# Kernel tuning notes

Measured on AMD Instinct MI355X. Metric: run time of the kernel, lower is better.

The kernel has to match this reference:

```python
import jax, jax.numpy as jnp
import numpy as np

B, H, S, DK = 4, 8, 2048, 64

def setup_inputs() -> dict:
    key = jax.random.key(0)
    kq, kk, kv = jax.random.split(key, 3)
    queries = jax.random.normal(kq, (B, H, S, DK), dtype=jnp.float32)
    keys = jax.random.normal(kk, (B, H, S, DK), dtype=jnp.float32)
    values = jax.random.normal(kv, (B, H, S, DK), dtype=jnp.float32)
    # causal mask: 1.0 where attention is disallowed (strictly upper triangular)
    mask = jnp.triu(jnp.ones((S, S), dtype=jnp.float32), k=1)[None, None]
    return {"queries": queries, "keys": keys, "values": values, "dk": DK, "mask": mask}

def reference(queries, keys, values, dk, mask):
    # score: [B, H, S, S]
    score = jnp.einsum("bhqd,bhkd->bhqk", queries, keys) / jnp.sqrt(jnp.float32(dk))
    if mask is not None:
        score = score + mask * -1e9
    attn = jax.nn.softmax(score, axis=-1)
    return jnp.einsum("bhqk,bhkd->bhqd", attn, values)
```

## Files before the change

### kernel.cpp

```cpp
#include <hip/hip_runtime.h>

typedef __attribute__((ext_vector_type(8))) short short8;
typedef __attribute__((ext_vector_type(4))) float f32x4;

#define DEV __device__ __forceinline__

constexpr int S_LEN = 2048;
constexpr int DK_LEN = 64;
constexpr int KBLK = 64;
constexpr float QSCALE = 0.18033688011112042f;

constexpr int KHI = 0;
constexpr int KLO = 8192;
constexpr int VHI = 16384;
constexpr int VLO = 24576;
constexpr int PBASE = 32768;
constexpr int LDS_BYTES = 65536;

DEV unsigned int f2bf(float x) {
  unsigned int u = __float_as_uint(x);
  return (u + 0x7fffu + ((u >> 16) & 1u)) >> 16;
}
DEV float bf2f(unsigned int h) { return __uint_as_float(h << 16); }
DEV int swz(int row, int slot) { return slot ^ ((row + (row >> 3)) & 7); }

DEV f32x4 MFMA(short8 a, short8 b, f32x4 c) {
  return __builtin_amdgcn_mfma_f32_16x16x32_bf16(a, b, c, 0, 0, 0);
}

__global__ __launch_bounds__(256, 2)
void fattn_fwd(const float* __restrict__ Qg, const float* __restrict__ Kg,
               const float* __restrict__ Vg, float* __restrict__ Og)
{
  __shared__ char smem[LDS_BYTES];
  const f32x4 vzero = {0.f, 0.f, 0.f, 0.f};
  const int tid = threadIdx.x;
  const int w  = tid >> 6;
  const int ln = tid & 63;
  const int g  = ln >> 4;
  const int c  = ln & 15;
  const int bh = blockIdx.y;
  const int j  = blockIdx.x;
  const int hc = 31 - j;
  const int lc = j;
  int qb[2];
  qb[0] = hc * 64 + 16 * w;
  qb[1] = lc * 64 + 16 * w;
  const size_t base = (size_t)bh * S_LEN * DK_LEN;
  const float* Qb = Qg + base;
  const float* Kb = Kg + base;
  const float* Vb = Vg + base;

  short8 qfh[2][2], qfl[2][2];
#pragma unroll
  for (int qt = 0; qt < 2; ++qt) {
    const float* Qr = Qb + (size_t)(qb[qt] + c) * DK_LEN;
#pragma unroll
    for (int kk = 0; kk < 2; ++kk) {
      f32x4 a = *(const f32x4*)(Qr + kk * 32 + 8 * g);
      f32x4 b = *(const f32x4*)(Qr + kk * 32 + 8 * g + 4);
      float x[8];
#pragma unroll
      for (int i = 0; i < 4; ++i) { x[i] = a[i] * QSCALE; x[4 + i] = b[i] * QSCALE; }
#pragma unroll
      for (int i = 0; i < 8; ++i) {
        unsigned int h = f2bf(x[i]);
        unsigned int l = f2bf(x[i] - bf2f(h));
        qfh[qt][kk][i] = (short)h;
        qfl[qt][kk][i] = (short)l;
      }
    }
  }

  f32x4 acc[4][2];
#pragma unroll
  for (int td = 0; td < 4; ++td)
#pragma unroll
    for (int qt = 0; qt < 2; ++qt) acc[td][qt] = vzero;
  float m_r[2]  = {-3e38f, -3e38f};
  float lsum[2] = {0.f, 0.f};
  f32x4 sv[2][4];
  char* pw = smem + PBASE + w * 8192;

  auto softmax_store = [&](int qt) {
    float mt = -3e38f;
#pragma unroll
    for (int t = 0; t < 4; ++t)
#pragma unroll
      for (int r = 0; r < 4; ++r) mt = fmaxf(mt, sv[qt][t][r]);
    mt = fmaxf(mt, __shfl_xor(mt, 16));
    mt = fmaxf(mt, __shfl_xor(mt, 32));
    float mn = fmaxf(m_r[qt], mt);
    float sc = exp2f(m_r[qt] - mn);
    m_r[qt] = mn;
#pragma unroll
    for (int td = 0; td < 4; ++td) acc[td][qt] *= sc;
    float ps = 0.f;
    int qrow = 16 * qt + c;
    char* ph = pw + qrow * 128;
    char* pl = ph + 4096;
#pragma unroll
    for (int t = 0; t < 4; ++t) {
      float p[4];
#pragma unroll
      for (int r = 0; r < 4; ++r) { p[r] = exp2f(sv[qt][t][r] - mn); ps += p[r]; }
      unsigned int h0 = f2bf(p[0]), h1 = f2bf(p[1]), h2 = f2bf(p[2]), h3 = f2bf(p[3]);
      unsigned int l0 = f2bf(p[0] - bf2f(h0)), l1 = f2bf(p[1] - bf2f(h1));
      unsigned int l2 = f2bf(p[2] - bf2f(h2)), l3 = f2bf(p[3] - bf2f(h3));
      int kb = 32 * t + 8 * g;
      int byte = swz(qrow, kb >> 4) * 16 + (kb & 15);
      *(unsigned int*)(ph + byte)     = h0 | (h1 << 16);
      *(unsigned int*)(ph + byte + 4) = h2 | (h3 << 16);
      *(unsigned int*)(pl + byte)     = l0 | (l1 << 16);
      *(unsigned int*)(pl + byte + 4) = l2 | (l3 << 16);
    }
    lsum[qt] = lsum[qt] * sc + ps;
  };

  const int ntiles = hc + 1;
  for (int kt = 0; kt < ntiles; ++kt) {
    const int kv0 = kt * KBLK;
    __syncthreads();
#pragma unroll
    for (int i = 0; i < 4; ++i) {
      int f = tid + 256 * i;
      int row = f >> 4, c4 = f & 15;
      f32x4 kv = *(const f32x4*)(Kb + (size_t)(kv0 + row) * DK_LEN + c4 * 4);
      unsigned int h[4], l[4];
#pragma unroll
      for (int jj = 0; jj < 4; ++jj) { h[jj] = f2bf(kv[jj]); l[jj] = f2bf(kv[jj] - bf2f(h[jj])); }
      int byte = row * 128 + swz(row, c4 >> 1) * 16 + (c4 & 1) * 8;
      *(uint2*)(smem + KHI + byte) = make_uint2(h[0] | (h[1] << 16), h[2] | (h[3] << 16));
      *(uint2*)(smem + KLO + byte) = make_uint2(l[0] | (l[1] << 16), l[2] | (l[3] << 16));
    }
#pragma unroll
    for (int it = 0; it < 2; ++it) {
      int p = tid + 256 * it;
      int rp = p >> 4, c4 = p & 15;
      const float* vp = Vb + (size_t)(kv0 + 2 * rp) * DK_LEN + c4 * 4;
      f32x4 v0 = *(const f32x4*)(vp);
      f32x4 v1 = *(const f32x4*)(vp + DK_LEN);
#pragma unroll
      for (int jj = 0; jj < 4; ++jj) {
        int d = 4 * c4 + jj;
        unsigned int h0 = f2bf(v0[jj]), h1 = f2bf(v1[jj]);
        unsigned int l0 = f2bf(v0[jj] - bf2f(h0)), l1 = f2bf(v1[jj] - bf2f(h1));
        int byte = d * 128 + swz(d, rp >> 2) * 16 + (rp & 3) * 4;
        *(unsigned int*)(smem + VHI + byte) = h0 | (h1 << 16);
        *(unsigned int*)(smem + VLO + byte) = l0 | (l1 << 16);
      }
    }
    __syncthreads();

    const bool act1 = (kv0 <= qb[1] + 15);
    const bool nm0  = (kv0 + KBLK - 1) > qb[0];
    const bool nm1  = (kv0 + KBLK - 1) > qb[1];

#pragma unroll
    for (int qt = 0; qt < 2; ++qt)
#pragma unroll
      for (int t = 0; t < 4; ++t) sv[qt][t] = vzero;
#pragma unroll
    for (int t = 0; t < 4; ++t) {
      int row = 16 * t + c;
#pragma unroll
      for (int kk = 0; kk < 2; ++kk) {
        int off = row * 128 + swz(row, 4 * kk + g) * 16;
        short8 kh = *(const short8*)(smem + KHI + off);
        short8 kl = *(const short8*)(smem + KLO + off);
        sv[0][t] = MFMA(kh, qfh[0][kk], sv[0][t]);
        sv[0][t] = MFMA(kh, qfl[0][kk], sv[0][t]);
        sv[0][t] = MFMA(kl, qfh[0][kk], sv[0][t]);
        if (act1) {
          sv[1][t] = MFMA(kh, qfh[1][kk], sv[1][t]);
          sv[1][t] = MFMA(kh, qfl[1][kk], sv[1][t]);
          sv[1][t] = MFMA(kl, qfh[1][kk], sv[1][t]);
        }
      }
    }
    if (nm0) {
      int q = qb[0] + c;
#pragma unroll
      for (int t = 0; t < 4; ++t)
#pragma unroll
        for (int r = 0; r < 4; ++r)
          if (kv0 + 16 * t + 4 * g + r > q) sv[0][t][r] = -1e38f;
    }
    if (act1 && nm1) {
      int q = qb[1] + c;
#pragma unroll
      for (int t = 0; t < 4; ++t)
#pragma unroll
        for (int r = 0; r < 4; ++r)
          if (kv0 + 16 * t + 4 * g + r > q) sv[1][t][r] = -1e38f;
    }

    softmax_store(0);
    if (act1) softmax_store(1);

    short8 pbh[2][2], pbl[2][2];
#pragma unroll
    for (int kk = 0; kk < 2; ++kk) {
      int qrow = c;
      int off = qrow * 128 + swz(qrow, 4 * kk + g) * 16;
      pbh[0][kk] = *(const short8*)(pw + off);
      pbl[0][kk] = *(const short8*)(pw + 4096 + off);
    }
    if (act1) {
#pragma unroll
      for (int kk = 0; kk < 2; ++kk) {
        int qrow = 16 + c;
        int off = qrow * 128 + swz(qrow, 4 * kk + g) * 16;
        pbh[1][kk] = *(const short8*)(pw + off);
        pbl[1][kk] = *(const short8*)(pw + 4096 + off);
      }
    }
#pragma unroll
    for (int td = 0; td < 4; ++td) {
      int d = 16 * td + c;
#pragma unroll
      for (int kk = 0; kk < 2; ++kk) {
        int off = d * 128 + swz(d, 4 * kk + g) * 16;
        short8 vh = *(const short8*)(smem + VHI + off);
        short8 vl = *(const short8*)(smem + VLO + off);
        acc[td][0] = MFMA(vh, pbh[0][kk], acc[td][0]);
        acc[td][0] = MFMA(vh, pbl[0][kk], acc[td][0]);
        acc[td][0] = MFMA(vl, pbh[0][kk], acc[td][0]);
        if (act1) {
          acc[td][1] = MFMA(vh, pbh[1][kk], acc[td][1]);
          acc[td][1] = MFMA(vh, pbl[1][kk], acc[td][1]);
          acc[td][1] = MFMA(vl, pbh[1][kk], acc[td][1]);
        }
      }
    }
  }

#pragma unroll
  for (int qt = 0; qt < 2; ++qt) {
    float l = lsum[qt];
    l += __shfl_xor(l, 16);
    l += __shfl_xor(l, 32);
    float inv = 1.f / l;
    float* Ob = Og + base + (size_t)(qb[qt] + c) * DK_LEN;
#pragma unroll
    for (int td = 0; td < 4; ++td) {
      f32x4 o = acc[td][qt] * inv;
      *(f32x4*)(Ob + 16 * td + 4 * g) = o;
    }
  }
}

extern "C" void kernel_launch(void* const* d_in, const int* in_sizes, int n_in,
                              void* d_out, int out_size, void* d_ws, size_t ws_size,
                              hipStream_t stream) {
  (void)in_sizes; (void)n_in; (void)d_ws; (void)ws_size; (void)out_size;
  const float* Q = (const float*)d_in[0];
  const float* K = (const float*)d_in[1];
  const float* V = (const float*)d_in[2];
  float* O = (float*)d_out;
  dim3 grid(16, 32);
  fattn_fwd<<<grid, dim3(256), 0, stream>>>(Q, K, V, O);
}
```

Before: 208.7 us.

## Precompute split-bf16 K/V tile images once and stream them into LDS

Adds a prep kernel that converts K and V once per call into swizzled hi/lo bf16 tile images in the workspace. The attention kernel then copies each 32KB tile straight into LDS with global_load_lds instead of converting fp32 K/V itself in every block. This removes the conversion work that each of the 16 query blocks per head was repeating. In exchange it costs an extra launch and a workspace write/read, and it only runs if the workspace is at least 32MB; otherwise the old path is used.

```diff
diff --git a/kernel.cpp b/kernel.cpp
--- a/kernel.cpp
+++ b/kernel.cpp
@@ -14,6 +14,7 @@
 constexpr int KLO = 8192;
 constexpr int VHI = 16384;
 constexpr int VLO = 24576;
+constexpr int TILE_IMG = 32768;
 constexpr int PBASE = 32768;
 constexpr int LDS_BYTES = 65536;
 
@@ -28,9 +29,61 @@
   return __builtin_amdgcn_mfma_f32_16x16x32_bf16(a, b, c, 0, 0, 0);
 }
 
+DEV void gload_lds16(const void* g, void* l) {
+  __builtin_amdgcn_global_load_lds(
+      (const __attribute__((address_space(1))) unsigned int*)g,
+      (__attribute__((address_space(3))) unsigned int*)l, 16, 0, 0);
+}
+
+__global__ __launch_bounds__(256)
+void prep_kv(const float* __restrict__ Kg, const float* __restrict__ Vg,
+             char* __restrict__ ws)
+{
+  const int tid = threadIdx.x;
+  const int kt  = blockIdx.x;
+  const int bh  = blockIdx.y;
+  const int kv0 = kt * KBLK;
+  const size_t base = (size_t)bh * S_LEN * DK_LEN;
+  const float* Kb = Kg + base;
+  const float* Vb = Vg + base;
+  char* wt = ws + ((size_t)bh * 32 + kt) * TILE_IMG;
+
+#pragma unroll
+  for (int i = 0; i < 4; ++i) {
+    int f = tid + 256 * i;
+    int row = f >> 4, c4 = f & 15;
+    f32x4 kv = *(const f32x4*)(Kb + (size_t)(kv0 + row) * DK_LEN + c4 * 4);
+    unsigned int h[4], l[4];
+#pragma unroll
+    for (int j = 0; j < 4; ++j) { h[j] = f2bf(kv[j]); l[j] = f2bf(kv[j] - bf2f(h[j])); }
+    int byte = row * 128 + swz(row, c4 >> 1) * 16 + (c4 & 1) * 8;
+    *(uint2*)(wt + KHI + byte) = make_uint2(h[0] | (h[1] << 16), h[2] | (h[3] << 16));
+    *(uint2*)(wt + KLO + byte) = make_uint2(l[0] | (l[1] << 16), l[2] | (l[3] << 16));
+  }
+#pragma unroll
+  for (int it = 0; it < 2; ++it) {
+    int p = tid + 256 * it;
+    int rp = p >> 4, c4 = p & 15;
+    const float* vp = Vb + (size_t)(kv0 + 2 * rp) * DK_LEN + c4 * 4;
+    f32x4 v0 = *(const f32x4*)(vp);
+    f32x4 v1 = *(const f32x4*)(vp + DK_LEN);
+#pragma unroll
+    for (int j = 0; j < 4; ++j) {
+      int d = 4 * c4 + j;
+      unsigned int h0 = f2bf(v0[j]), h1 = f2bf(v1[j]);
+      unsigned int l0 = f2bf(v0[j] - bf2f(h0)), l1 = f2bf(v1[j] - bf2f(h1));
+      int byte = d * 128 + swz(d, rp >> 2) * 16 + (rp & 3) * 4;
+      *(unsigned int*)(wt + VHI + byte) = h0 | (h1 << 16);
+      *(unsigned int*)(wt + VLO + byte) = l0 | (l1 << 16);
+    }
+  }
+}
+
+template<bool PRE>
 __global__ __launch_bounds__(256, 2)
 void fattn_fwd(const float* __restrict__ Qg, const float* __restrict__ Kg,
-               const float* __restrict__ Vg, float* __restrict__ Og)
+               const float* __restrict__ Vg, float* __restrict__ Og,
+               const char* __restrict__ ws)
 {
   __shared__ char smem[LDS_BYTES];
   const f32x4 vzero = {0.f, 0.f, 0.f, 0.f};
@@ -50,6 +103,7 @@
   const float* Qb = Qg + base;
   const float* Kb = Kg + base;
   const float* Vb = Vg + base;
+  const char* wsb = ws + (size_t)bh * 32 * TILE_IMG;
 
   short8 qfh[2][2], qfl[2][2];
 #pragma unroll
@@ -121,33 +175,40 @@
   for (int kt = 0; kt < ntiles; ++kt) {
     const int kv0 = kt * KBLK;
     __syncthreads();
-#pragma unroll
-    for (int i = 0; i < 4; ++i) {
-      int f = tid + 256 * i;
-      int row = f >> 4, c4 = f & 15;
-      f32x4 kv = *(const f32x4*)(Kb + (size_t)(kv0 + row) * DK_LEN + c4 * 4);
-      unsigned int h[4], l[4];
-#pragma unroll
-      for (int jj = 0; jj < 4; ++jj) { h[jj] = f2bf(kv[jj]); l[jj] = f2bf(kv[jj] - bf2f(h[jj])); }
-      int byte = row * 128 + swz(row, c4 >> 1) * 16 + (c4 & 1) * 8;
-      *(uint2*)(smem + KHI + byte) = make_uint2(h[0] | (h[1] << 16), h[2] | (h[3] << 16));
-      *(uint2*)(smem + KLO + byte) = make_uint2(l[0] | (l[1] << 16), l[2] | (l[3] << 16));
-    }
-#pragma unroll
-    for (int it = 0; it < 2; ++it) {
-      int p = tid + 256 * it;
-      int rp = p >> 4, c4 = p & 15;
-      const float* vp = Vb + (size_t)(kv0 + 2 * rp) * DK_LEN + c4 * 4;
-      f32x4 v0 = *(const f32x4*)(vp);
-      f32x4 v1 = *(const f32x4*)(vp + DK_LEN);
-#pragma unroll
-      for (int jj = 0; jj < 4; ++jj) {
-        int d = 4 * c4 + jj;
-        unsigned int h0 = f2bf(v0[jj]), h1 = f2bf(v1[jj]);
-        unsigned int l0 = f2bf(v0[jj] - bf2f(h0)), l1 = f2bf(v1[jj] - bf2f(h1));
-        int byte = d * 128 + swz(d, rp >> 2) * 16 + (rp & 3) * 4;
-        *(unsigned int*)(smem + VHI + byte) = h0 | (h1 << 16);
-        *(unsigned int*)(smem + VLO + byte) = l0 | (l1 << 16);
+    if constexpr (PRE) {
+      const char* wt = wsb + (size_t)kt * TILE_IMG;
+#pragma unroll
+      for (int i = 0; i < 8; ++i)
+        gload_lds16(wt + i * 4096 + tid * 16, smem + i * 4096 + w * 1024);
+    } else {
+#pragma unroll
+      for (int i = 0; i < 4; ++i) {
+        int f = tid + 256 * i;
+        int row = f >> 4, c4 = f & 15;
+        f32x4 kv = *(const f32x4*)(Kb + (size_t)(kv0 + row) * DK_LEN + c4 * 4);
+        unsigned int h[4], l[4];
+#pragma unroll
+        for (int jj = 0; jj < 4; ++jj) { h[jj] = f2bf(kv[jj]); l[jj] = f2bf(kv[jj] - bf2f(h[jj])); }
+        int byte = row * 128 + swz(row, c4 >> 1) * 16 + (c4 & 1) * 8;
+        *(uint2*)(smem + KHI + byte) = make_uint2(h[0] | (h[1] << 16), h[2] | (h[3] << 16));
+        *(uint2*)(smem + KLO + byte) = make_uint2(l[0] | (l[1] << 16), l[2] | (l[3] << 16));
+      }
+#pragma unroll
+      for (int it = 0; it < 2; ++it) {
+        int p = tid + 256 * it;
+        int rp = p >> 4, c4 = p & 15;
+        const float* vp = Vb + (size_t)(kv0 + 2 * rp) * DK_LEN + c4 * 4;
+        f32x4 v0 = *(const f32x4*)(vp);
+        f32x4 v1 = *(const f32x4*)(vp + DK_LEN);
+#pragma unroll
+        for (int jj = 0; jj < 4; ++jj) {
+          int d = 4 * c4 + jj;
+          unsigned int h0 = f2bf(v0[jj]), h1 = f2bf(v1[jj]);
+          unsigned int l0 = f2bf(v0[jj] - bf2f(h0)), l1 = f2bf(v1[jj] - bf2f(h1));
+          int byte = d * 128 + swz(d, rp >> 2) * 16 + (rp & 3) * 4;
+          *(unsigned int*)(smem + VHI + byte) = h0 | (h1 << 16);
+          *(unsigned int*)(smem + VLO + byte) = l0 | (l1 << 16);
+        }
       }
     }
     __syncthreads();
@@ -201,8 +262,7 @@
     short8 pbh[2][2], pbl[2][2];
 #pragma unroll
     for (int kk = 0; kk < 2; ++kk) {
-      int qrow = c;
-      int off = qrow * 128 + swz(qrow, 4 * kk + g) * 16;
+      int off = c * 128 + swz(c, 4 * kk + g) * 16;
       pbh[0][kk] = *(const short8*)(pw + off);
       pbl[0][kk] = *(const short8*)(pw + 4096 + off);
     }
@@ -253,11 +313,17 @@
 extern "C" void kernel_launch(void* const* d_in, const int* in_sizes, int n_in,
                               void* d_out, int out_size, void* d_ws, size_t ws_size,
                               hipStream_t stream) {
-  (void)in_sizes; (void)n_in; (void)d_ws; (void)ws_size; (void)out_size;
+  (void)in_sizes; (void)n_in; (void)out_size;
   const float* Q = (const float*)d_in[0];
   const float* K = (const float*)d_in[1];
   const float* V = (const float*)d_in[2];
   float* O = (float*)d_out;
   dim3 grid(16, 32);
-  fattn_fwd<<<grid, dim3(256), 0, stream>>>(Q, K, V, O);
-}
+  const size_t WS_NEED = (size_t)32 * 32 * TILE_IMG;
+  if (ws_size >= WS_NEED) {
+    prep_kv<<<dim3(32, 32), 256, 0, stream>>>(K, V, (char*)d_ws);
+    fattn_fwd<true><<<grid, dim3(256), 0, stream>>>(Q, K, V, O, (const char*)d_ws);
+  } else {
+    fattn_fwd<false><<<grid, dim3(256), 0, stream>>>(Q, K, V, O, (const char*)d_ws);
+  }
+}
```

New measurement: 204.5 us. 2.0% less time.
